# Optimization experiments

Hardware: AMD Instinct MI355X
Metric: run time of the kernel (lower is better)

Reference implementation:

```python
import jax, jax.numpy as jnp
import numpy as np

N_NODES = 50000
N_EDGES = 800000
IN_FEATS = 128
H_FEATS = 128
NUM_CLASSES = 64


def _linear_params(key, fan_in, fan_out):
    kw, kb = jax.random.split(key)
    bound = 1.0 / np.sqrt(fan_in)
    W = jax.random.uniform(kw, (fan_out, fan_in), minval=-bound, maxval=bound, dtype=jnp.float32)
    b = jax.random.uniform(kb, (fan_out,), minval=-bound, maxval=bound, dtype=jnp.float32)
    return W, b


def setup_inputs() -> dict:
    key = jax.random.key(0)
    k_feat, k_src, k_dst, k1, k2, k3 = jax.random.split(key, 6)
    in_feat = jax.random.normal(k_feat, (N_NODES, IN_FEATS), dtype=jnp.float32)
    src = jax.random.randint(k_src, (N_EDGES,), 0, N_NODES, dtype=jnp.int32)
    dst = jax.random.randint(k_dst, (N_EDGES,), 0, N_NODES, dtype=jnp.int32)
    W1, b1 = _linear_params(k1, IN_FEATS, H_FEATS)
    W2, b2 = _linear_params(k2, H_FEATS, H_FEATS)
    W3, b3 = _linear_params(k3, H_FEATS, NUM_CLASSES)
    return {"in_feat": in_feat, "W1": W1, "b1": b1, "W2": W2, "b2": b2,
            "W3": W3, "b3": b3, "src": src, "dst": dst}


def reference(in_feat, W1, b1, W2, b2, W3, b3, src, dst):
    N = in_feat.shape[0]

    def gin_layer(x, W, b):
        # DGL GINConv with eps=0: (x + sum of in-neighbor messages) -> Linear
        agg = jax.ops.segment_sum(x[src], dst, num_segments=N)  # [N, d]
        return jax.nn.relu((x + agg) @ W.T + b)

    h = gin_layer(in_feat, W1, b1)
    h = gin_layer(h, W2, b2)
    h = gin_layer(h, W3, b3)
    return h
```

## Files before the change

kernel.cpp:

```cpp
#include <hip/hip_runtime.h>

typedef _Float16 half8 __attribute__((ext_vector_type(8)));
typedef _Float16 half2v __attribute__((ext_vector_type(2)));
typedef float floatx4 __attribute__((ext_vector_type(4)));
typedef unsigned int uintx4 __attribute__((ext_vector_type(4)));

union AB { uint4 u; half8 h; };
union H2 { unsigned int u; _Float16 h[2]; };
union H2P { unsigned int u; half2v h; };
union US16 { uintx4 u[2]; unsigned short s[16]; };

#define CAPLOG 6
#define CAP 64

__global__ __launch_bounds__(256) void histA_init_k(
    const int* __restrict__ dst, int* __restrict__ histG, int E, int nbins,
    const float* __restrict__ F, const float* __restrict__ W1,
    const float* __restrict__ W2, const float* __restrict__ W3,
    _Float16* __restrict__ hX, _Float16* __restrict__ W1h,
    _Float16* __restrict__ W2h, _Float16* __restrict__ W3h,
    _Float16* __restrict__ hZ,
    int n4f, int n4w1, int n4w2, int n4w3, int zoffX4, int zoffZ4) {
    int t = threadIdx.x;
    if (blockIdx.x < 256) {
        __shared__ int h[256];
        h[t] = 0;
        __syncthreads();
        int per = (E + 255) / 256;
        int beg = blockIdx.x * per;
        int end = min(E, beg + per);
        for (int e = beg + t; e < end; e += 256)
            atomicAdd(&h[dst[e] >> 8], 1);
        __syncthreads();
        for (int i = t; i < nbins; i += 256)
            histG[i * 256 + blockIdx.x] = h[i];
        return;
    }
    int i = (blockIdx.x - 256) * 256 + t;
    const float* X;
    _Float16* O;
    int j;
    if (i < n4f) { X = F; O = hX; j = i; }
    else if (i < n4f + n4w1) { X = W1; O = W1h; j = i - n4f; }
    else if (i < n4f + n4w1 + n4w2) { X = W2; O = W2h; j = i - n4f - n4w1; }
    else if (i < n4f + n4w1 + n4w2 + n4w3) { X = W3; O = W3h; j = i - n4f - n4w1 - n4w2; }
    else {
        int z = i - (n4f + n4w1 + n4w2 + n4w3);
        if (z < 16) ((uint4*)hX)[zoffX4 + z] = make_uint4(0, 0, 0, 0);
        else if (z < 24) ((uint4*)hZ)[zoffZ4 + (z - 16)] = make_uint4(0, 0, 0, 0);
        return;
    }
    float4 v = reinterpret_cast<const float4*>(X)[j];
    union { uint2 u; _Float16 h[4]; } o;
    o.h[0] = (_Float16)v.x; o.h[1] = (_Float16)v.y;
    o.h[2] = (_Float16)v.z; o.h[3] = (_Float16)v.w;
    reinterpret_cast<uint2*>(O)[j] = o.u;
}

__global__ __launch_bounds__(1024) void scan1_k(const int* __restrict__ x,
                                                int* __restrict__ inc,
                                                int* __restrict__ partial, int n) {
    __shared__ int sd[1024];
    int t = threadIdx.x;
    int v = blockIdx.x * 1024 + t;
    sd[t] = (v < n) ? x[v] : 0;
    __syncthreads();
    for (int off = 1; off < 1024; off <<= 1) {
        int val = (t >= off) ? sd[t - off] : 0;
        __syncthreads();
        sd[t] += val;
        __syncthreads();
    }
    if (v < n) inc[v] = sd[t];
    if (t == 1023) partial[blockIdx.x] = sd[1023];
}

__global__ __launch_bounds__(256) void scatterB_k(const int* __restrict__ src,
                                                  const int* __restrict__ dst,
                                                  const int* __restrict__ inc,
                                                  const int* __restrict__ histG,
                                                  const int* __restrict__ partial, int nparts,
                                                  unsigned int* __restrict__ binned,
                                                  int E, int nbins) {
    __shared__ int cur[256];
    __shared__ int pp[64];
    int t = threadIdx.x, blk = blockIdx.x;
    if (t < 64) {
        int v = (t < nparts) ? partial[t] : 0;
        for (int off = 1; off < 64; off <<= 1) {
            int n = __shfl_up(v, off, 64);
            if (t >= off) v += n;
        }
        int ex = __shfl_up(v, 1, 64);
        if (t == 0) ex = 0;
        pp[t] = ex;
    }
    __syncthreads();
    for (int i = t; i < nbins; i += 256) {
        int idx = i * 256 + blk;
        cur[i] = inc[idx] + pp[idx >> 10] - histG[idx];
    }
    __syncthreads();
    int per = (E + 255) / 256;
    int beg = blk * per;
    int end = min(E, beg + per);
    for (int e = beg + t; e < end; e += 256) {
        int d = dst[e];
        int s = src[e];
        int pos = atomicAdd(&cur[d >> 8], 1);
        binned[pos] = ((unsigned int)(d & 255) << 16) | (unsigned int)s;
    }
}

__global__ __launch_bounds__(256) void binB_k(const unsigned int* __restrict__ binned,
                                              const int* __restrict__ inc,
                                              const int* __restrict__ histG,
                                              const int* __restrict__ partial, int nparts,
                                              unsigned short* __restrict__ col,
                                              int* __restrict__ cnt,
                                              int N, int E, int nbins) {
    __shared__ unsigned short lcol[256 * CAP];
    __shared__ int lcnt[256];
    __shared__ int pp[64];
    __shared__ int bounds[2];
    int t = threadIdx.x;
    int b = blockIdx.x;
    if (t < 64) {
        int v = (t < nparts) ? partial[t] : 0;
        for (int off = 1; off < 64; off <<= 1) {
            int n = __shfl_up(v, off, 64);
            if (t >= off) v += n;
        }
        int ex = __shfl_up(v, 1, 64);
        if (t == 0) ex = 0;
        pp[t] = ex;
    }
    unsigned int* lcol32 = (unsigned int*)lcol;
    for (int i = t; i < 256 * CAP / 2; i += 256) lcol32[i] = 0xFFFFFFFFu;
    lcnt[t] = 0;
    __syncthreads();
    if (t == 0) {
        int i0 = b * 256;
        bounds[0] = inc[i0] + pp[i0 >> 10] - histG[i0];
    } else if (t == 1) {
        if (b == nbins - 1) bounds[1] = E;
        else {
            int i1 = (b + 1) * 256;
            bounds[1] = inc[i1] + pp[i1 >> 10] - histG[i1];
        }
    }
    __syncthreads();
    int beg = bounds[0], end = bounds[1];
    for (int e = beg + t; e < end; e += 256) {
        unsigned int u = binned[e];
        int dl = u >> 16;
        int pos = atomicAdd(&lcnt[dl], 1);
        if (pos < CAP) lcol[(dl << CAPLOG) + pos] = (unsigned short)(u & 0xFFFFu);
    }
    __syncthreads();
    int base = b << 8;
    int nodes = min(256, N - base);
    uint4* colg = (uint4*)(col + ((size_t)base << CAPLOG));
    const uint4* coll = (const uint4*)lcol;
    for (int i = t; i < nodes * 8; i += 256) colg[i] = coll[i];
    for (int i = t; i < nodes; i += 256) cnt[base + i] = lcnt[i];
}

__global__ __launch_bounds__(256) void aggregate_k(const _Float16* __restrict__ X,
                                                   const int* __restrict__ cnt,
                                                   const unsigned short* __restrict__ col,
                                                   _Float16* __restrict__ Y,
                                                   int nnodes) {
    int w = blockIdx.x * 4 + (threadIdx.x >> 6);
    int lane = threadIdx.x & 63;
    if (w >= nnodes) return;
    const unsigned int* X32 = reinterpret_cast<const unsigned int*>(X);
    int deg = cnt[w];
    if (deg > CAP) deg = CAP;
    int degp = (deg + 15) & ~15;
    const unsigned short* c = col + ((size_t)w << CAPLOG);

    H2P acc[16];
#pragma unroll
    for (int j = 0; j < 16; j++) acc[j].u = 0u;

    for (int e = 0; e < degp; e += 16) {
        US16 ix;
        ix.u[0] = *reinterpret_cast<const uintx4*>(c + e);
        ix.u[1] = *reinterpret_cast<const uintx4*>(c + e + 8);
        H2P u[16];
#pragma unroll
        for (int j = 0; j < 16; j++) {
            int s = (int)ix.s[j];
            s = (s < nnodes) ? s : nnodes;
            u[j].u = X32[(size_t)s * 64 + lane];
        }
#pragma unroll
        for (int j = 0; j < 16; j++) acc[j].h += u[j].h;
    }

    float s0 = 0.f, s1 = 0.f;
#pragma unroll
    for (int j = 0; j < 16; j++) {
        s0 += (float)acc[j].h[0];
        s1 += (float)acc[j].h[1];
    }
    H2 xs, r;
    xs.u = X32[(size_t)w * 64 + lane];
    r.h[0] = (_Float16)((float)xs.h[0] + s0);
    r.h[1] = (_Float16)((float)xs.h[1] + s1);
    __builtin_nontemporal_store(r.u, reinterpret_cast<unsigned int*>(Y) + (size_t)w * 64 + lane);
}

__global__ __launch_bounds__(256) void agg_final_k(const _Float16* __restrict__ Z,
                                                   const int* __restrict__ cnt,
                                                   const unsigned short* __restrict__ col,
                                                   const float* __restrict__ bias,
                                                   float* __restrict__ out, int nnodes) {
    int lane = threadIdx.x & 63;
    int fl = lane & 31;
    int node = blockIdx.x * 8 + (threadIdx.x >> 6) * 2 + (lane >> 5);
    if (node >= nnodes) return;
    const unsigned int* Z32 = (const unsigned int*)Z;

    int deg = cnt[node];
    if (deg > CAP) deg = CAP;
    int degp = (deg + 15) & ~15;
    const unsigned short* c = col + ((size_t)node << CAPLOG);

    H2P acc[16];
#pragma unroll
    for (int j = 0; j < 16; j++) acc[j].u = 0u;

    for (int e = 0; e < degp; e += 16) {
        US16 ix;
        ix.u[0] = *reinterpret_cast<const uintx4*>(c + e);
        ix.u[1] = *reinterpret_cast<const uintx4*>(c + e + 8);
        H2P u[16];
#pragma unroll
        for (int j = 0; j < 16; j++) {
            int s = (int)ix.s[j];
            s = (s < nnodes) ? s : nnodes;
            u[j].u = Z32[(size_t)s * 32 + fl];
        }
#pragma unroll
        for (int j = 0; j < 16; j++) acc[j].h += u[j].h;
    }

    float s0 = 0.f, s1 = 0.f;
#pragma unroll
    for (int j = 0; j < 16; j++) {
        s0 += (float)acc[j].h[0];
        s1 += (float)acc[j].h[1];
    }
    H2 xs;
    xs.u = Z32[(size_t)node * 32 + fl];
    float2 bv = reinterpret_cast<const float2*>(bias)[fl];
    float2 r;
    r.x = fmaxf((float)xs.h[0] + s0 + bv.x, 0.f);
    r.y = fmaxf((float)xs.h[1] + s1 + bv.y, 0.f);
    reinterpret_cast<float2*>(out)[(size_t)node * 32 + fl] = r;
}

__global__ __launch_bounds__(256) void gemm_mfma_k(const _Float16* __restrict__ Y,
                                                   const _Float16* __restrict__ Wh,
                                                   const float* __restrict__ bias,
                                                   _Float16* __restrict__ out, int nnodes) {
    constexpr int NT = 8;
    constexpr int WSTR = 136;
    __shared__ _Float16 Wl[128 * WSTR];
    __shared__ float Bl[128];

    const int t = threadIdx.x;
    for (int p = t; p < 128 * 16; p += 256) {
        int f = p >> 4;
        int kq = (p & 15) * 8;
        *reinterpret_cast<uint4*>(&Wl[f * WSTR + kq]) =
            *reinterpret_cast<const uint4*>(Wh + f * 128 + kq);
    }
    if (t < 128) Bl[t] = bias[t];
    __syncthreads();

    const int wave = t >> 6;
    const int lane = t & 63;
    const int quad = lane >> 4;
    const int fcol = lane & 15;
    const int m_base = (blockIdx.x * 4 + wave) * 16;
    const int row = m_base + fcol;
    const bool rowok = row < nnodes;

    floatx4 acc[NT];
#pragma unroll
    for (int ft = 0; ft < NT; ft++) acc[ft] = (floatx4){0.f, 0.f, 0.f, 0.f};

    const uint4* Yrow = reinterpret_cast<const uint4*>(Y + (size_t)row * 128);
#pragma unroll
    for (int step = 0; step < 4; step++) {
        AB a;
        if (rowok) a.u = Yrow[step * 4 + quad];
        else       a.u = make_uint4(0u, 0u, 0u, 0u);
#pragma unroll
        for (int ft = 0; ft < NT; ft++) {
            half8 b = *reinterpret_cast<const half8*>(
                &Wl[(ft * 16 + fcol) * WSTR + step * 32 + quad * 8]);
            acc[ft] = __builtin_amdgcn_mfma_f32_16x16x32_f16(a.h, b, acc[ft], 0, 0, 0);
        }
    }

#pragma unroll
    for (int ft = 0; ft < NT; ft++) {
        int f = ft * 16 + fcol;
        float bv = Bl[f];
#pragma unroll
        for (int r = 0; r < 4; r++) {
            int node = m_base + quad * 4 + r;
            if (node < nnodes)
                out[(size_t)node * 128 + f] = (_Float16)fmaxf(acc[ft][r] + bv, 0.f);
        }
    }
}

__global__ __launch_bounds__(256) void gemm23_k(const _Float16* __restrict__ Y,
                                                const _Float16* __restrict__ W2h,
                                                const float* __restrict__ b2,
                                                const _Float16* __restrict__ W3h,
                                                _Float16* __restrict__ hZ, int nnodes) {
    constexpr int WSTR = 136;
    __shared__ _Float16 Wl[128 * WSTR];
    __shared__ _Float16 Hl[64 * WSTR];
    __shared__ float Bl[128];

    const int t = threadIdx.x;
    for (int p = t; p < 128 * 16; p += 256) {
        int f = p >> 4;
        int kq = (p & 15) * 8;
        *reinterpret_cast<uint4*>(&Wl[f * WSTR + kq]) =
            *reinterpret_cast<const uint4*>(W2h + f * 128 + kq);
    }
    if (t < 128) Bl[t] = b2[t];
    __syncthreads();

    const int wave = t >> 6;
    const int lane = t & 63;
    const int quad = lane >> 4;
    const int fcol = lane & 15;
    const int m_base = (blockIdx.x * 4 + wave) * 16;
    const int row = m_base + fcol;
    const bool rowok = row < nnodes;

    floatx4 acc[8];
#pragma unroll
    for (int ft = 0; ft < 8; ft++) acc[ft] = (floatx4){0.f, 0.f, 0.f, 0.f};

    const uint4* Yrow = reinterpret_cast<const uint4*>(Y + (size_t)row * 128);
#pragma unroll
    for (int step = 0; step < 4; step++) {
        AB a;
        if (rowok) a.u = Yrow[step * 4 + quad];
        else       a.u = make_uint4(0u, 0u, 0u, 0u);
#pragma unroll
        for (int ft = 0; ft < 8; ft++) {
            half8 b = *reinterpret_cast<const half8*>(
                &Wl[(ft * 16 + fcol) * WSTR + step * 32 + quad * 8]);
            acc[ft] = __builtin_amdgcn_mfma_f32_16x16x32_f16(a.h, b, acc[ft], 0, 0, 0);
        }
    }

#pragma unroll
    for (int ft = 0; ft < 8; ft++) {
        int f = ft * 16 + fcol;
        float bv = Bl[f];
#pragma unroll
        for (int r = 0; r < 4; r++) {
            int nl = wave * 16 + quad * 4 + r;
            Hl[nl * WSTR + f] = (_Float16)fmaxf(acc[ft][r] + bv, 0.f);
        }
    }
    __syncthreads();

    for (int p = t; p < 64 * 16; p += 256) {
        int f = p >> 4;
        int kq = (p & 15) * 8;
        *reinterpret_cast<uint4*>(&Wl[f * WSTR + kq]) =
            *reinterpret_cast<const uint4*>(W3h + f * 128 + kq);
    }
    __syncthreads();

    floatx4 acc2[4];
#pragma unroll
    for (int ft = 0; ft < 4; ft++) acc2[ft] = (floatx4){0.f, 0.f, 0.f, 0.f};
#pragma unroll
    for (int step = 0; step < 4; step++) {
        AB a;
        a.h = *reinterpret_cast<const half8*>(
            &Hl[(wave * 16 + fcol) * WSTR + step * 32 + quad * 8]);
#pragma unroll
        for (int ft = 0; ft < 4; ft++) {
            half8 b = *reinterpret_cast<const half8*>(
                &Wl[(ft * 16 + fcol) * WSTR + step * 32 + quad * 8]);
            acc2[ft] = __builtin_amdgcn_mfma_f32_16x16x32_f16(a.h, b, acc2[ft], 0, 0, 0);
        }
    }
#pragma unroll
    for (int ft = 0; ft < 4; ft++) {
        int f = ft * 16 + fcol;
#pragma unroll
        for (int r = 0; r < 4; r++) {
            int node = m_base + quad * 4 + r;
            if (node < nnodes)
                hZ[(size_t)node * 64 + f] = (_Float16)acc2[ft][r];
        }
    }
}

extern "C" void kernel_launch(void* const* d_in, const int* in_sizes, int n_in,
                              void* d_out, int out_size, void* d_ws, size_t ws_size,
                              hipStream_t stream) {
    const float* in_feat = (const float*)d_in[0];
    const float* W1 = (const float*)d_in[1];
    const float* b1 = (const float*)d_in[2];
    const float* W2 = (const float*)d_in[3];
    const float* b2 = (const float*)d_in[4];
    const float* W3 = (const float*)d_in[5];
    const float* b3 = (const float*)d_in[6];
    const int* src = (const int*)d_in[7];
    const int* dst = (const int*)d_in[8];
    float* out = (float*)d_out;

    const int N = in_sizes[0] / 128;
    const int E = in_sizes[7];
    const int szW1 = in_sizes[1];
    const int szW2 = in_sizes[3];
    const int szW3 = in_sizes[5];
    const int nbins = (N + 255) >> 8;
    const int nhist = nbins * 256;

    char* p = (char*)d_ws;
    int* cnt = (int*)p;               p += (size_t)N * 4;
    unsigned short* col = (unsigned short*)p; p += (size_t)N * CAP * 2;
    int* histG = (int*)p;             p += (size_t)nhist * 4;
    int* incS = (int*)p;              p += (size_t)nhist * 4;
    int* partial = (int*)p;           p += 256;
    unsigned int* binned = (unsigned int*)p; p += (size_t)E * 4;
    _Float16* hX = (_Float16*)p;      p += (size_t)(N + 1) * 128 * 2;
    _Float16* hB = (_Float16*)p;      p += (size_t)N * 128 * 2;
    _Float16* hZ = (_Float16*)p;      p += (size_t)(N + 1) * 64 * 2;
    _Float16* W1h = (_Float16*)p;     p += (size_t)szW1 * 2;
    _Float16* W2h = (_Float16*)p;     p += (size_t)szW2 * 2;
    _Float16* W3h = (_Float16*)p;     p += (size_t)szW3 * 2;

    const int nblk_scan = (nhist + 1023) / 1024;

    {
        int n4f = N * 128 / 4;
        int total = n4f + szW1 / 4 + szW2 / 4 + szW3 / 4 + 32;
        int iblk = (total + 255) / 256;
        histA_init_k<<<256 + iblk, 256, 0, stream>>>(dst, histG, E, nbins,
                                                     in_feat, W1, W2, W3,
                                                     hX, W1h, W2h, W3h, hZ,
                                                     n4f, szW1 / 4, szW2 / 4, szW3 / 4,
                                                     N * 16, N * 8);
    }
    scan1_k<<<nblk_scan, 1024, 0, stream>>>(histG, incS, partial, nhist);
    scatterB_k<<<256, 256, 0, stream>>>(src, dst, incS, histG, partial, nblk_scan,
                                        binned, E, nbins);
    binB_k<<<nbins, 256, 0, stream>>>(binned, incS, histG, partial, nblk_scan,
                                      col, cnt, N, E, nbins);

    const int nblk_agg = (N + 3) / 4;
    const int nblk_gemm = (N + 63) / 64;
    aggregate_k<<<nblk_agg, 256, 0, stream>>>(hX, cnt, col, hB, N);
    gemm_mfma_k<<<nblk_gemm, 256, 0, stream>>>(hB, W1h, b1, hX, N);
    aggregate_k<<<nblk_agg, 256, 0, stream>>>(hX, cnt, col, hB, N);
    gemm23_k<<<nblk_gemm, 256, 0, stream>>>(hB, W2h, b2, W3h, hZ, N);
    agg_final_k<<<(N + 7) / 8, 256, 0, stream>>>(hZ, cnt, col, b3, out, N);
}
```

Before: 229.2 us.

## Reorder layer 1 to transform before aggregating and drop input conversion pass

Layer 1 now runs the linear transform first, reading fp32 features and converting them to half inside the GEMM. It then aggregates the transformed rows and applies bias and ReLU, using linearity to get (x+agg)W = xW + agg(xW). This removes the separate fp32-to-half conversion pass over the input features. It also fuses bias and ReLU into the aggregation instead of the GEMM epilogue. The cost is an extra buffer, and rounding changes because aggregation now sums transformed values in fp16.

```diff
diff --git a/kernel.cpp b/kernel.cpp
--- a/kernel.cpp
+++ b/kernel.cpp
@@ -15,12 +15,10 @@
 
 __global__ __launch_bounds__(256) void histA_init_k(
     const int* __restrict__ dst, int* __restrict__ histG, int E, int nbins,
-    const float* __restrict__ F, const float* __restrict__ W1,
-    const float* __restrict__ W2, const float* __restrict__ W3,
-    _Float16* __restrict__ hX, _Float16* __restrict__ W1h,
-    _Float16* __restrict__ W2h, _Float16* __restrict__ W3h,
-    _Float16* __restrict__ hZ,
-    int n4f, int n4w1, int n4w2, int n4w3, int zoffX4, int zoffZ4) {
+    const float* __restrict__ W1, const float* __restrict__ W2, const float* __restrict__ W3,
+    _Float16* __restrict__ W1h, _Float16* __restrict__ W2h, _Float16* __restrict__ W3h,
+    _Float16* __restrict__ z1, _Float16* __restrict__ h1, _Float16* __restrict__ hZ,
+    int n4w1, int n4w2, int n4w3, int zoff128, int zoff64) {
     int t = threadIdx.x;
     if (blockIdx.x < 256) {
         __shared__ int h[256];
@@ -40,14 +38,14 @@
     const float* X;
     _Float16* O;
     int j;
-    if (i < n4f) { X = F; O = hX; j = i; }
-    else if (i < n4f + n4w1) { X = W1; O = W1h; j = i - n4f; }
-    else if (i < n4f + n4w1 + n4w2) { X = W2; O = W2h; j = i - n4f - n4w1; }
-    else if (i < n4f + n4w1 + n4w2 + n4w3) { X = W3; O = W3h; j = i - n4f - n4w1 - n4w2; }
+    if (i < n4w1) { X = W1; O = W1h; j = i; }
+    else if (i < n4w1 + n4w2) { X = W2; O = W2h; j = i - n4w1; }
+    else if (i < n4w1 + n4w2 + n4w3) { X = W3; O = W3h; j = i - n4w1 - n4w2; }
     else {
-        int z = i - (n4f + n4w1 + n4w2 + n4w3);
-        if (z < 16) ((uint4*)hX)[zoffX4 + z] = make_uint4(0, 0, 0, 0);
-        else if (z < 24) ((uint4*)hZ)[zoffZ4 + (z - 16)] = make_uint4(0, 0, 0, 0);
+        int z = i - (n4w1 + n4w2 + n4w3);
+        if (z < 16) ((uint4*)z1)[zoff128 + z] = make_uint4(0, 0, 0, 0);
+        else if (z < 32) ((uint4*)h1)[zoff128 + (z - 16)] = make_uint4(0, 0, 0, 0);
+        else if (z < 40) ((uint4*)hZ)[zoff64 + (z - 32)] = make_uint4(0, 0, 0, 0);
         return;
     }
     float4 v = reinterpret_cast<const float4*>(X)[j];
@@ -166,6 +164,112 @@
     for (int i = t; i < nodes; i += 256) cnt[base + i] = lcnt[i];
 }
 
+__global__ __launch_bounds__(256) void gemm_z1_k(const float* __restrict__ X,
+                                                 const _Float16* __restrict__ Wh,
+                                                 _Float16* __restrict__ z1, int nnodes) {
+    constexpr int WSTR = 136;
+    __shared__ _Float16 Wl[128 * WSTR];
+
+    const int t = threadIdx.x;
+    for (int p = t; p < 128 * 16; p += 256) {
+        int f = p >> 4;
+        int kq = (p & 15) * 8;
+        *reinterpret_cast<uint4*>(&Wl[f * WSTR + kq]) =
+            *reinterpret_cast<const uint4*>(Wh + f * 128 + kq);
+    }
+    __syncthreads();
+
+    const int wave = t >> 6;
+    const int lane = t & 63;
+    const int quad = lane >> 4;
+    const int fcol = lane & 15;
+    const int m_base = (blockIdx.x * 4 + wave) * 16;
+    const int row = m_base + fcol;
+    const bool rowok = row < nnodes;
+
+    floatx4 acc[8];
+#pragma unroll
+    for (int ft = 0; ft < 8; ft++) acc[ft] = (floatx4){0.f, 0.f, 0.f, 0.f};
+
+    const float* Xrow = X + (size_t)row * 128;
+#pragma unroll
+    for (int step = 0; step < 4; step++) {
+        AB a;
+        if (rowok) {
+            float4 f0 = *reinterpret_cast<const float4*>(Xrow + step * 32 + quad * 8);
+            float4 f1 = *reinterpret_cast<const float4*>(Xrow + step * 32 + quad * 8 + 4);
+            a.h[0] = (_Float16)f0.x; a.h[1] = (_Float16)f0.y;
+            a.h[2] = (_Float16)f0.z; a.h[3] = (_Float16)f0.w;
+            a.h[4] = (_Float16)f1.x; a.h[5] = (_Float16)f1.y;
+            a.h[6] = (_Float16)f1.z; a.h[7] = (_Float16)f1.w;
+        } else a.u = make_uint4(0u, 0u, 0u, 0u);
+#pragma unroll
+        for (int ft = 0; ft < 8; ft++) {
+            half8 b = *reinterpret_cast<const half8*>(
+                &Wl[(ft * 16 + fcol) * WSTR + step * 32 + quad * 8]);
+            acc[ft] = __builtin_amdgcn_mfma_f32_16x16x32_f16(a.h, b, acc[ft], 0, 0, 0);
+        }
+    }
+
+#pragma unroll
+    for (int ft = 0; ft < 8; ft++) {
+        int f = ft * 16 + fcol;
+#pragma unroll
+        for (int r = 0; r < 4; r++) {
+            int node = m_base + quad * 4 + r;
+            if (node < nnodes)
+                z1[(size_t)node * 128 + f] = (_Float16)acc[ft][r];
+        }
+    }
+}
+
+__global__ __launch_bounds__(256) void agg_z1_k(const _Float16* __restrict__ Z,
+                                                const int* __restrict__ cnt,
+                                                const unsigned short* __restrict__ col,
+                                                const float* __restrict__ bias,
+                                                _Float16* __restrict__ H, int nnodes) {
+    int w = blockIdx.x * 4 + (threadIdx.x >> 6);
+    int lane = threadIdx.x & 63;
+    if (w >= nnodes) return;
+    const unsigned int* Z32 = reinterpret_cast<const unsigned int*>(Z);
+    int deg = cnt[w];
+    if (deg > CAP) deg = CAP;
+    int degp = (deg + 15) & ~15;
+    const unsigned short* c = col + ((size_t)w << CAPLOG);
+
+    H2P acc[16];
+#pragma unroll
+    for (int j = 0; j < 16; j++) acc[j].u = 0u;
+
+    for (int e = 0; e < degp; e += 16) {
+        US16 ix;
+        ix.u[0] = *reinterpret_cast<const uintx4*>(c + e);
+        ix.u[1] = *reinterpret_cast<const uintx4*>(c + e + 8);
+        H2P u[16];
+#pragma unroll
+        for (int j = 0; j < 16; j++) {
+            int s = (int)ix.s[j];
+            s = (s < nnodes) ? s : nnodes;
+            u[j].u = Z32[(size_t)s * 64 + lane];
+        }
+#pragma unroll
+        for (int j = 0; j < 16; j++) acc[j].h += u[j].h;
+    }
+
+    float s0 = 0.f, s1 = 0.f;
+#pragma unroll
+    for (int j = 0; j < 16; j++) {
+        s0 += (float)acc[j].h[0];
+        s1 += (float)acc[j].h[1];
+    }
+    float2 bv = reinterpret_cast<const float2*>(bias)[lane];
+    H2 xs, r;
+    xs.u = Z32[(size_t)w * 64 + lane];
+    r.h[0] = (_Float16)fmaxf((float)xs.h[0] + s0 + bv.x, 0.f);
+    r.h[1] = (_Float16)fmaxf((float)xs.h[1] + s1 + bv.y, 0.f);
+    __builtin_nontemporal_store(r.u, reinterpret_cast<unsigned int*>(H) + (size_t)w * 64 + lane);
+}
+
 __global__ __launch_bounds__(256) void aggregate_k(const _Float16* __restrict__ X,
                                                    const int* __restrict__ cnt,
                                                    const unsigned short* __restrict__ col,
@@ -262,64 +366,6 @@
     reinterpret_cast<float2*>(out)[(size_t)node * 32 + fl] = r;
 }
 
-__global__ __launch_bounds__(256) void gemm_mfma_k(const _Float16* __restrict__ Y,
-                                                   const _Float16* __restrict__ Wh,
-                                                   const float* __restrict__ bias,
-                                                   _Float16* __restrict__ out, int nnodes) {
-    constexpr int NT = 8;
-    constexpr int WSTR = 136;
-    __shared__ _Float16 Wl[128 * WSTR];
-    __shared__ float Bl[128];
-
-    const int t = threadIdx.x;
-    for (int p = t; p < 128 * 16; p += 256) {
-        int f = p >> 4;
-        int kq = (p & 15) * 8;
-        *reinterpret_cast<uint4*>(&Wl[f * WSTR + kq]) =
-            *reinterpret_cast<const uint4*>(Wh + f * 128 + kq);
-    }
-    if (t < 128) Bl[t] = bias[t];
-    __syncthreads();
-
-    const int wave = t >> 6;
-    const int lane = t & 63;
-    const int quad = lane >> 4;
-    const int fcol = lane & 15;
-    const int m_base = (blockIdx.x * 4 + wave) * 16;
-    const int row = m_base + fcol;
-    const bool rowok = row < nnodes;
-
-    floatx4 acc[NT];
-#pragma unroll
-    for (int ft = 0; ft < NT; ft++) acc[ft] = (floatx4){0.f, 0.f, 0.f, 0.f};
-
-    const uint4* Yrow = reinterpret_cast<const uint4*>(Y + (size_t)row * 128);
-#pragma unroll
-    for (int step = 0; step < 4; step++) {
-        AB a;
-        if (rowok) a.u = Yrow[step * 4 + quad];
-        else       a.u = make_uint4(0u, 0u, 0u, 0u);
-#pragma unroll
-        for (int ft = 0; ft < NT; ft++) {
-            half8 b = *reinterpret_cast<const half8*>(
-                &Wl[(ft * 16 + fcol) * WSTR + step * 32 + quad * 8]);
-            acc[ft] = __builtin_amdgcn_mfma_f32_16x16x32_f16(a.h, b, acc[ft], 0, 0, 0);
-        }
-    }
-
-#pragma unroll
-    for (int ft = 0; ft < NT; ft++) {
-        int f = ft * 16 + fcol;
-        float bv = Bl[f];
-#pragma unroll
-        for (int r = 0; r < 4; r++) {
-            int node = m_base + quad * 4 + r;
-            if (node < nnodes)
-                out[(size_t)node * 128 + f] = (_Float16)fmaxf(acc[ft][r] + bv, 0.f);
-        }
-    }
-}
-
 __global__ __launch_bounds__(256) void gemm23_k(const _Float16* __restrict__ Y,
                                                 const _Float16* __restrict__ W2h,
                                                 const float* __restrict__ b2,
@@ -442,7 +488,8 @@
     int* incS = (int*)p;              p += (size_t)nhist * 4;
     int* partial = (int*)p;           p += 256;
     unsigned int* binned = (unsigned int*)p; p += (size_t)E * 4;
-    _Float16* hX = (_Float16*)p;      p += (size_t)(N + 1) * 128 * 2;
+    _Float16* z1 = (_Float16*)p;      p += (size_t)(N + 1) * 128 * 2;
+    _Float16* h1 = (_Float16*)p;      p += (size_t)(N + 1) * 128 * 2;
     _Float16* hB = (_Float16*)p;      p += (size_t)N * 128 * 2;
     _Float16* hZ = (_Float16*)p;      p += (size_t)(N + 1) * 64 * 2;
     _Float16* W1h = (_Float16*)p;     p += (size_t)szW1 * 2;
@@ -452,13 +499,12 @@
     const int nblk_scan = (nhist + 1023) / 1024;
 
     {
-        int n4f = N * 128 / 4;
-        int total = n4f + szW1 / 4 + szW2 / 4 + szW3 / 4 + 32;
+        int total = szW1 / 4 + szW2 / 4 + szW3 / 4 + 40;
         int iblk = (total + 255) / 256;
         histA_init_k<<<256 + iblk, 256, 0, stream>>>(dst, histG, E, nbins,
-                                                     in_feat, W1, W2, W3,
-                                                     hX, W1h, W2h, W3h, hZ,
-                                                     n4f, szW1 / 4, szW2 / 4, szW3 / 4,
+                                                     W1, W2, W3, W1h, W2h, W3h,
+                                                     z1, h1, hZ,
+                                                     szW1 / 4, szW2 / 4, szW3 / 4,
                                                      N * 16, N * 8);
     }
     scan1_k<<<nblk_scan, 1024, 0, stream>>>(histG, incS, partial, nhist);
@@ -469,9 +515,9 @@
 
     const int nblk_agg = (N + 3) / 4;
     const int nblk_gemm = (N + 63) / 64;
-    aggregate_k<<<nblk_agg, 256, 0, stream>>>(hX, cnt, col, hB, N);
-    gemm_mfma_k<<<nblk_gemm, 256, 0, stream>>>(hB, W1h, b1, hX, N);
-    aggregate_k<<<nblk_agg, 256, 0, stream>>>(hX, cnt, col, hB, N);
+    gemm_z1_k<<<nblk_gemm, 256, 0, stream>>>(in_feat, W1h, z1, N);
+    agg_z1_k<<<nblk_agg, 256, 0, stream>>>(z1, cnt, col, b1, h1, N);
+    aggregate_k<<<nblk_agg, 256, 0, stream>>>(h1, cnt, col, hB, N);
     gemm23_k<<<nblk_gemm, 256, 0, stream>>>(hB, W2h, b2, W3h, hZ, N);
     agg_final_k<<<(N + 7) / 8, 256, 0, stream>>>(hZ, cnt, col, b3, out, N);
 }
```

Result: faster. 220.2 us (-3.9%).
